# Kernel optimization log

Hardware: AMD Instinct MI355X
Metric: run time of the kernel (lower is better)

## Reference

```python
import jax, jax.numpy as jnp
import numpy as np

CODEBOOK_SIZE = 1024
CODEBOOK_DIM = 64
COMMITMENT_WEIGHT = 0.25
DECAY = 0.99
EPS = 1e-5


def setup_inputs() -> dict:
    key = jax.random.key(0)
    k1, k2, k3 = jax.random.split(key, 3)
    B, D, T = 32, CODEBOOK_DIM, 4096
    z = jax.random.normal(k1, (B, D, T), dtype=jnp.float32)
    embedding = jax.random.normal(k2, (CODEBOOK_SIZE, CODEBOOK_DIM), dtype=jnp.float32)
    cluster_size = jnp.zeros((CODEBOOK_SIZE,), dtype=jnp.float32)
    embed_avg = jax.random.normal(k3, (CODEBOOK_SIZE, CODEBOOK_DIM), dtype=jnp.float32)
    return {"z": z, "embedding": embedding, "cluster_size": cluster_size, "embed_avg": embed_avg}


def reference(z, embedding, cluster_size, embed_avg):
    # z: [B, D, T]; embedding/embed_avg: [K, D]; cluster_size: [K]
    B, D, T = z.shape
    K = embedding.shape[0]
    z_flat = jnp.transpose(z, (0, 2, 1)).reshape(-1, D)  # [N, D], N = B*T

    # squared-euclidean distances via expansion (matches torch cdist expansion)
    dist = (
        jnp.sum(z_flat * z_flat, axis=1, keepdims=True)
        + jnp.sum(embedding * embedding, axis=1)
        - 2.0 * (z_flat @ embedding.T)
    )  # [N, K]
    indices = jnp.argmin(dist, axis=1)  # [N] int

    # EMA updates (training path). one_hot.sum(0) -> segment count; one_hot.T @ z_flat -> segment sum
    counts = jax.ops.segment_sum(jnp.ones(z_flat.shape[0], dtype=z_flat.dtype), indices, num_segments=K)
    new_cluster_size = cluster_size * DECAY + (1.0 - DECAY) * counts
    embed_sum = jax.ops.segment_sum(z_flat, indices, num_segments=K)  # [K, D]
    new_embed_avg = embed_avg * DECAY + (1.0 - DECAY) * embed_sum
    n = jnp.sum(new_cluster_size)
    smoothed = (new_cluster_size + EPS) / (n + K * EPS) * n  # Laplace smoothing
    new_embedding = new_embed_avg / smoothed[:, None]  # [K, D]

    # quantize with the *updated* codebook (as in the torch in-place update)
    z_q_flat = new_embedding[indices]  # [N, D] gather
    loss = COMMITMENT_WEIGHT * jnp.mean((z_flat - jax.lax.stop_gradient(z_q_flat)) ** 2)
    # straight-through estimator
    z_q_flat = z_flat + jax.lax.stop_gradient(z_q_flat - z_flat)
    z_q = jnp.transpose(z_q_flat.reshape(B, T, D), (0, 2, 1))  # [B, D, T]
    return z_q, loss, indices.reshape(B, T)
```

## Files before the change

### kernel.cpp

```cpp
#include <hip/hip_runtime.h>

#define N_PTS 131072
#define TD 4096
#define DD 64
#define KK 1024
#define MARGIN_TH 2e-3f

typedef short bf16x8 __attribute__((ext_vector_type(8)));
typedef float f32x4  __attribute__((ext_vector_type(4)));

__device__ inline unsigned short f2bf(float f) {
    unsigned u = __float_as_uint(f);
    unsigned r = u + 0x7FFFu + ((u >> 16) & 1u);
    return (unsigned short)(r >> 16);
}
__device__ inline float bf2f(unsigned short h) {
    return __uint_as_float(((unsigned)h) << 16);
}

__device__ inline void gload_lds16(const unsigned short* g, unsigned short* l) {
    __builtin_amdgcn_global_load_lds(
        (const __attribute__((address_space(1))) unsigned int*)g,
        (__attribute__((address_space(3))) unsigned int*)l, 16, 0, 0);
}

__global__ __launch_bounds__(256) void vq_prep(const float* __restrict__ z,
                                               unsigned short* __restrict__ zh,
                                               unsigned short* __restrict__ zl)
{
    __shared__ float tile[64][65];
    const int tid = threadIdx.x;
    const int b = blockIdx.x >> 6;
    const int t0 = (blockIdx.x & 63) * 64;

    const int d = tid >> 2, tq = tid & 3;
#pragma unroll
    for (int it = 0; it < 4; ++it) {
        const int tt = tq * 16 + it * 4;
        const float4 v = *(const float4*)(z + ((size_t)b * DD + d) * TD + t0 + tt);
        tile[d][tt] = v.x; tile[d][tt + 1] = v.y; tile[d][tt + 2] = v.z; tile[d][tt + 3] = v.w;
    }
    __syncthreads();

    const int p = tid >> 2, dg = tid & 3;
    bf16x8 h0, h1, l0, l1;
#pragma unroll
    for (int j = 0; j < 8; ++j) {
        const float v0 = -tile[dg * 16 + j][p];
        const unsigned short a = f2bf(v0);
        h0[j] = (short)a; l0[j] = (short)f2bf(v0 - bf2f(a));
        const float v1 = -tile[dg * 16 + 8 + j][p];
        const unsigned short c = f2bf(v1);
        h1[j] = (short)c; l1[j] = (short)f2bf(v1 - bf2f(c));
    }
    const size_t o = ((size_t)(b * TD + t0 + p)) * DD + dg * 16;
    *(bf16x8*)(zh + o) = h0;
    *(bf16x8*)(zh + o + 8) = h1;
    *(bf16x8*)(zl + o) = l0;
    *(bf16x8*)(zl + o + 8) = l1;
}

__global__ __launch_bounds__(256) void vq_eprep(const float* __restrict__ emb,
                                                unsigned short* __restrict__ efh,
                                                unsigned short* __restrict__ efl,
                                                float* __restrict__ halfnorm)
{
    const int k = blockIdx.x * 256 + threadIdx.x;
    if (k >= KK) return;
    const int t = k >> 4, col = k & 15;
    const float* e = emb + (size_t)k * DD;
    double s = 0.0;
#pragma unroll
    for (int d = 0; d < DD; ++d) {
        const float v = e[d];
        const double dv = (double)v;
        s = fma(dv, dv, s);
        const unsigned short h = f2bf(v);
        const int q = d >> 3, j = d & 7;
        const size_t pos = (size_t)t * 1024 + (q >> 2) * 512 + ((q & 3) * 16 + col) * 8 + j;
        efh[pos] = h;
        efl[pos] = f2bf(v - bf2f(h));
    }
    halfnorm[k] = (float)(0.5 * s);
}

__global__ __launch_bounds__(256, 4) void vq_screen_mfma(
    const unsigned short* __restrict__ zh, const unsigned short* __restrict__ zl,
    const unsigned short* __restrict__ efh, const unsigned short* __restrict__ efl,
    const float* __restrict__ hn,
    int* __restrict__ idx_ws, float* __restrict__ ind_out,
    int* __restrict__ nflag, int* __restrict__ flags, int* __restrict__ hist)
{
    __shared__ __align__(16) unsigned short tiles[4][2048];
    __shared__ float hns[KK];

    const int tid  = threadIdx.x;
    const int lane = tid & 63;
    const int wv   = tid >> 6;
    const int quad = lane >> 4;
    const int col  = lane & 15;
    const int loff = lane * 8;
    const int pbase = blockIdx.x * 128 + wv * 32;

    const bf16x8* pA0h = (const bf16x8*)(zh + (size_t)(pbase + col) * DD + quad * 8);
    const bf16x8* pA0l = (const bf16x8*)(zl + (size_t)(pbase + col) * DD + quad * 8);
    const bf16x8* pA1h = (const bf16x8*)(zh + (size_t)(pbase + 16 + col) * DD + quad * 8);
    const bf16x8* pA1l = (const bf16x8*)(zl + (size_t)(pbase + 16 + col) * DD + quad * 8);
    const bf16x8 A0h0 = pA0h[0], A0h1 = pA0h[4];
    const bf16x8 A0l0 = pA0l[0], A0l1 = pA0l[4];
    const bf16x8 A1h0 = pA1h[0], A1h1 = pA1h[4];
    const bf16x8 A1l0 = pA1l[0], A1l1 = pA1l[4];

    ((float4*)hns)[tid] = ((const float4*)hn)[tid];

    const unsigned short* sgl = (wv < 2 ? efh : efl) + (tid & 127) * 8;

    asm volatile("s_waitcnt vmcnt(0)" ::: "memory");
    __builtin_amdgcn_sched_barrier(0);
    __syncthreads();

#define SCREEN_STAGE(T) gload_lds16(sgl + (size_t)(T) * 1024, &tiles[(T) & 3][tid * 8])

    SCREEN_STAGE(0);
    SCREEN_STAGE(1);

    float best0[4]  = {1e30f, 1e30f, 1e30f, 1e30f};
    float best20[4] = {1e30f, 1e30f, 1e30f, 1e30f};
    int   bidx0[4]  = {0, 0, 0, 0};
    float best1[4]  = {1e30f, 1e30f, 1e30f, 1e30f};
    float best21[4] = {1e30f, 1e30f, 1e30f, 1e30f};
    int   bidx1[4]  = {0, 0, 0, 0};

#define SCREEN_BODY(T)                                                              \
    {                                                                               \
        const unsigned short* buf = &tiles[(T) & 3][0];                             \
        const bf16x8 Bh0 = *(const bf16x8*)(buf + loff);                            \
        const bf16x8 Bh1 = *(const bf16x8*)(buf + 512 + loff);                      \
        const bf16x8 Bl0 = *(const bf16x8*)(buf + 1024 + loff);                     \
        const bf16x8 Bl1 = *(const bf16x8*)(buf + 1536 + loff);                     \
        const float chn = hns[(T) * 16 + col];                                      \
        f32x4 a0 = {chn, chn, chn, chn};                                            \
        f32x4 a1 = {chn, chn, chn, chn};                                            \
        a0 = __builtin_amdgcn_mfma_f32_16x16x32_bf16(A0h0, Bh0, a0, 0, 0, 0);       \
        a1 = __builtin_amdgcn_mfma_f32_16x16x32_bf16(A1h0, Bh0, a1, 0, 0, 0);       \
        a0 = __builtin_amdgcn_mfma_f32_16x16x32_bf16(A0h1, Bh1, a0, 0, 0, 0);       \
        a1 = __builtin_amdgcn_mfma_f32_16x16x32_bf16(A1h1, Bh1, a1, 0, 0, 0);       \
        a0 = __builtin_amdgcn_mfma_f32_16x16x32_bf16(A0l0, Bh0, a0, 0, 0, 0);       \
        a1 = __builtin_amdgcn_mfma_f32_16x16x32_bf16(A1l0, Bh0, a1, 0, 0, 0);       \
        a0 = __builtin_amdgcn_mfma_f32_16x16x32_bf16(A0l1, Bh1, a0, 0, 0, 0);       \
        a1 = __builtin_amdgcn_mfma_f32_16x16x32_bf16(A1l1, Bh1, a1, 0, 0, 0);       \
        a0 = __builtin_amdgcn_mfma_f32_16x16x32_bf16(A0h0, Bl0, a0, 0, 0, 0);       \
        a1 = __builtin_amdgcn_mfma_f32_16x16x32_bf16(A1h0, Bl0, a1, 0, 0, 0);       \
        a0 = __builtin_amdgcn_mfma_f32_16x16x32_bf16(A0h1, Bl1, a0, 0, 0, 0);       \
        a1 = __builtin_amdgcn_mfma_f32_16x16x32_bf16(A1h1, Bl1, a1, 0, 0, 0);       \
        const int code = (T) * 16 + col;                                            \
        _Pragma("unroll")                                                           \
        for (int r = 0; r < 4; ++r) {                                               \
            const float s0 = a0[r];                                                 \
            best20[r] = __builtin_amdgcn_fmed3f(best0[r], best20[r], s0);           \
            if (s0 < best0[r]) { best0[r] = s0; bidx0[r] = code; }                  \
            const float s1 = a1[r];                                                 \
            best21[r] = __builtin_amdgcn_fmed3f(best1[r], best21[r], s1);           \
            if (s1 < best1[r]) { best1[r] = s1; bidx1[r] = code; }                  \
        }                                                                           \
    }

    for (int t = 0; t < 62; ++t) {
        SCREEN_STAGE(t + 2);
        asm volatile("s_waitcnt vmcnt(2)" ::: "memory");
        __builtin_amdgcn_sched_barrier(0);
        __builtin_amdgcn_s_barrier();
        __builtin_amdgcn_sched_barrier(0);
        SCREEN_BODY(t);
    }
    asm volatile("s_waitcnt vmcnt(1)" ::: "memory");
    __builtin_amdgcn_sched_barrier(0);
    __builtin_amdgcn_s_barrier();
    __builtin_amdgcn_sched_barrier(0);
    SCREEN_BODY(62);
    asm volatile("s_waitcnt vmcnt(0)" ::: "memory");
    __builtin_amdgcn_sched_barrier(0);
    __builtin_amdgcn_s_barrier();
    __builtin_amdgcn_sched_barrier(0);
    SCREEN_BODY(63);

#undef SCREEN_STAGE
#undef SCREEN_BODY

#pragma unroll
    for (int off = 1; off < 16; off <<= 1) {
#pragma unroll
        for (int r = 0; r < 4; ++r) {
            {
                const float ob  = __shfl_xor(best0[r],  off, 64);
                const float ob2 = __shfl_xor(best20[r], off, 64);
                const int   oi  = __shfl_xor(bidx0[r],  off, 64);
                const float nb2 = fminf(fminf(best20[r], ob2), fmaxf(best0[r], ob));
                if (ob < best0[r]) { best0[r] = ob; bidx0[r] = oi; }
                best20[r] = nb2;
            }
            {
                const float ob  = __shfl_xor(best1[r],  off, 64);
                const float ob2 = __shfl_xor(best21[r], off, 64);
                const int   oi  = __shfl_xor(bidx1[r],  off, 64);
                const float nb2 = fminf(fminf(best21[r], ob2), fmaxf(best1[r], ob));
                if (ob < best1[r]) { best1[r] = ob; bidx1[r] = oi; }
                best21[r] = nb2;
            }
        }
    }

    if (col == 0) {
#pragma unroll
        for (int r = 0; r < 4; ++r) {
            const int n0 = pbase + quad * 4 + r;
            idx_ws[n0] = bidx0[r];
            ind_out[n0] = (float)bidx0[r];
            atomicAdd(&hist[bidx0[r]], 1);
            if (best20[r] - best0[r] < MARGIN_TH) {
                const int pos = atomicAdd(nflag, 1);
                flags[pos] = n0;
            }
            const int n1 = pbase + 16 + quad * 4 + r;
            idx_ws[n1] = bidx1[r];
            ind_out[n1] = (float)bidx1[r];
            atomicAdd(&hist[bidx1[r]], 1);
            if (best21[r] - best1[r] < MARGIN_TH) {
                const int pos = atomicAdd(nflag, 1);
                flags[pos] = n1;
            }
        }
    }
}

__global__ __launch_bounds__(256) void vq_fallback(
    const float* __restrict__ z, const float* __restrict__ emb,
    int* __restrict__ idx_ws, float* __restrict__ ind_out,
    const int* __restrict__ nflag, const int* __restrict__ flags,
    int* __restrict__ hist)
{
    __shared__ float zs[4][DD];
    const int total = *nflag;
    const int lane = threadIdx.x & 63;
    const int wid = threadIdx.x >> 6;
    const int gw = blockIdx.x * 4 + wid;

    for (int i = gw; i < total; i += gridDim.x * 4) {
        const int n = flags[i];
        const int b = n >> 12, t = n & 4095;
        zs[wid][lane] = z[((size_t)b * DD + lane) * TD + t];
        __builtin_amdgcn_s_waitcnt(0);
        double best = 1e300;
        int bi = KK;
        for (int kc = 0; kc < KK / 64; ++kc) {
            const int k = kc * 64 + lane;
            const float4* e = (const float4*)(emb + (size_t)k * DD);
            double dot = 0.0, nn = 0.0;
#pragma unroll
            for (int j = 0; j < 16; ++j) {
                float4 ev = e[j];
                double e0 = (double)ev.x, e1 = (double)ev.y, e2 = (double)ev.z, e3 = (double)ev.w;
                nn = fma(e0, e0, fma(e1, e1, fma(e2, e2, fma(e3, e3, nn))));
                dot = fma((double)zs[wid][4 * j + 0], e0,
                      fma((double)zs[wid][4 * j + 1], e1,
                      fma((double)zs[wid][4 * j + 2], e2,
                      fma((double)zs[wid][4 * j + 3], e3, dot))));
            }
            double s = 0.5 * nn - dot;
            if (s < best || (s == best && k < bi)) { best = s; bi = k; }
        }
        for (int off = 32; off > 0; off >>= 1) {
            double os = __shfl_down(best, off, 64);
            int oi = __shfl_down(bi, off, 64);
            if (os < best || (os == best && oi < bi)) { best = os; bi = oi; }
        }
        if (lane == 0) {
            const int old = idx_ws[n];
            if (bi != old) {
                idx_ws[n] = bi;
                ind_out[n] = (float)bi;
                atomicAdd(&hist[old], -1);
                atomicAdd(&hist[bi], 1);
            }
        }
    }
}

__global__ __launch_bounds__(1024) void vq_prefix_smo(
    const int* __restrict__ hist, const float* __restrict__ cs,
    int* __restrict__ cursor, float* __restrict__ rsmo)
{
    __shared__ int tmp[KK];
    __shared__ double dred[KK];
    const int k = threadIdx.x;
    const int c = hist[k];
    tmp[k] = c;
    const double ncs = 0.99 * (double)cs[k] + 0.01 * (double)c;
    dred[k] = ncs;
    __syncthreads();
    for (int off = 1; off < KK; off <<= 1) {
        int u = (k >= off) ? tmp[k - off] : 0;
        __syncthreads();
        tmp[k] += u;
        __syncthreads();
    }
    cursor[k] = tmp[k] - c;
    for (int s = 512; s > 0; s >>= 1) {
        if (k < s) dred[k] += dred[k + s];
        __syncthreads();
    }
    const double nsum = dred[0];
    const double smo = (ncs + 1e-5) / (nsum + (double)KK * 1e-5) * nsum;
    rsmo[k] = (float)(1.0 / smo);
}

__global__ __launch_bounds__(256) void vq_scatter(const int* __restrict__ idx_ws,
                                                  int* __restrict__ cursor, int* __restrict__ order)
{
    const int n = blockIdx.x * 256 + threadIdx.x;
    const int bi = idx_ws[n];
    const int pos = atomicAdd(&cursor[bi], 1);
    order[pos] = n;
}

__global__ __launch_bounds__(256) void vq_esum2(
    const unsigned short* __restrict__ zh, const unsigned short* __restrict__ zl,
    const int* __restrict__ idx_ws, const int* __restrict__ order,
    float* __restrict__ esum)
{
    const int tid = threadIdx.x;
    const int lane = tid & 63;
    const int w = tid >> 6;
    const int base = blockIdx.x * 256 + w * 64;

    const int pid_l = order[base + lane];
    const int code_l = idx_ws[pid_l];

    float v[64];
#pragma unroll
    for (int j = 0; j < 64; ++j) {
        const int pj = __shfl(pid_l, j, 64);
        const size_t o = (size_t)pj * DD + lane;
        v[j] = bf2f(zh[o]) + bf2f(zl[o]);
    }

    float racc = 0.f;
    int cur = __shfl(code_l, 0, 64);
#pragma unroll
    for (int j = 0; j < 64; ++j) {
        const int cj = __shfl(code_l, j, 64);
        if (cj != cur) {
            atomicAdd(&esum[(size_t)cur * DD + lane], -racc);
            racc = 0.f;
            cur = cj;
        }
        racc += v[j];
    }
    atomicAdd(&esum[(size_t)cur * DD + lane], -racc);
}

__global__ __launch_bounds__(256) void vq_newE(
    const float* __restrict__ avg, const float* __restrict__ esum,
    const float* __restrict__ rsmo, float* __restrict__ newE)
{
    const int j = blockIdx.x * 256 + threadIdx.x;
    newE[j] = (float)((0.99 * (double)avg[j] + 0.01 * (double)esum[j]) * (double)rsmo[j >> 6]);
}

__global__ __launch_bounds__(256) void vq_gather_loss(
    const float* __restrict__ z, const float* __restrict__ newE,
    const int* __restrict__ idx_ws, float* __restrict__ zq_out,
    double* __restrict__ loss_acc, int* __restrict__ done_cnt,
    float* __restrict__ loss_out)
{
    const int tid = threadIdx.x;
    const int n = blockIdx.x * 256 + tid;
    const int b = n >> 12;
    const int t = n & 4095;
    const float* zb = z + ((size_t)b * DD) * TD + t;
    float* ob = zq_out + ((size_t)b * DD) * TD + t;
    const int bi = idx_ws[n];
    const float* e = newE + (size_t)bi * DD;
    double acc = 0.0;
#pragma unroll
    for (int d = 0; d < DD; ++d) {
        float q = e[d];
        float zv = zb[(size_t)d * TD];
        ob[(size_t)d * TD] = q;
        float df = zv - q;
        acc = fma((double)df, (double)df, acc);
    }
    for (int off = 32; off > 0; off >>= 1) acc += __shfl_down(acc, off, 64);
    __shared__ double wsum[4];
    const int wid = tid >> 6, lane = tid & 63;
    if (lane == 0) wsum[wid] = acc;
    __syncthreads();
    if (tid == 0) {
        atomicAdd(loss_acc, wsum[0] + wsum[1] + wsum[2] + wsum[3]);
        __threadfence();
        const int prev = atomicAdd(done_cnt, 1);
        if (prev == gridDim.x - 1) {
            __threadfence();
            *loss_out = (float)(0.25 * (*loss_acc) / (double)(N_PTS * DD));
        }
    }
}

extern "C" void kernel_launch(void* const* d_in, const int* in_sizes, int n_in,
                              void* d_out, int out_size, void* d_ws, size_t ws_size,
                              hipStream_t stream) {
    const float* z    = (const float*)d_in[0];
    const float* emb  = (const float*)d_in[1];
    const float* cs   = (const float*)d_in[2];
    const float* avg  = (const float*)d_in[3];

    float* out      = (float*)d_out;
    float* zq_out   = out;
    float* loss_out = out + 8388608;
    float* ind_out  = out + 8388609;

    unsigned short* zh = (unsigned short*)d_out;
    unsigned short* zl = (unsigned short*)((char*)d_out + 16777216);

    char* ws = (char*)d_ws;
    int*            idx_ws   = (int*)ws;
    float*          newE     = (float*)(ws + 524288);
    float*          esum     = (float*)(ws + 786432);
    int*            hist     = (int*)(ws + 1048576);
    int*            nflag    = (int*)(ws + 1052672);
    int*            done_cnt = (int*)(ws + 1052676);
    double*         loss_acc = (double*)(ws + 1052680);
    float*          halfnorm = (float*)(ws + 1052688);
    int*            cursor   = (int*)(ws + 1056784);
    int*            flags    = (int*)(ws + 1060880);
    int*            order    = (int*)(ws + 1585168);
    unsigned short* efh      = (unsigned short*)(ws + 2109456);
    unsigned short* efl      = (unsigned short*)(ws + 2240528);
    float*          rsmo     = (float*)(ws + 2371600);

    hipMemsetAsync(ws + 786432, 0, 266256, stream);

    vq_prep<<<2048, 256, 0, stream>>>(z, zh, zl);
    vq_eprep<<<4, 256, 0, stream>>>(emb, efh, efl, halfnorm);
    vq_screen_mfma<<<1024, 256, 0, stream>>>(zh, zl, efh, efl, halfnorm,
                                             idx_ws, ind_out, nflag, flags, hist);
    vq_fallback<<<128, 256, 0, stream>>>(z, emb, idx_ws, ind_out, nflag, flags, hist);
    vq_prefix_smo<<<1, 1024, 0, stream>>>(hist, cs, cursor, rsmo);
    vq_scatter<<<N_PTS / 256, 256, 0, stream>>>(idx_ws, cursor, order);
    vq_esum2<<<N_PTS / 256, 256, 0, stream>>>(zh, zl, idx_ws, order, esum);
    vq_newE<<<256, 256, 0, stream>>>(avg, esum, rsmo, newE);
    vq_gather_loss<<<N_PTS / 256, 256, 0, stream>>>(z, newE, idx_ws, zq_out,
                                                    loss_acc, done_cnt, loss_out);
}
```

Before: 342.6 us.

## Merge codebook prep into z prep and build histogram in a separate pass

The codebook prep kernel is folded into vq_prep as four extra blocks, which removes one launch. Those blocks also save the half-norms in double precision, so the fallback no longer recomputes the codebook norms. Per-point global histogram atomics are taken out of the screen and fallback kernels. A new shared-memory histogram kernel runs after the fallback instead. The screen argmin update becomes branchless, and the fallback grid grows from 128 to 1024 blocks. The cost is one extra launch, and dnn shares its workspace region with newE, which is safe only if newE is written after the fallback finishes.

```diff
diff --git a/kernel.cpp b/kernel.cpp
--- a/kernel.cpp
+++ b/kernel.cpp
@@ -26,10 +26,37 @@
 
 __global__ __launch_bounds__(256) void vq_prep(const float* __restrict__ z,
                                                unsigned short* __restrict__ zh,
-                                               unsigned short* __restrict__ zl)
+                                               unsigned short* __restrict__ zl,
+                                               const float* __restrict__ emb,
+                                               unsigned short* __restrict__ efh,
+                                               unsigned short* __restrict__ efl,
+                                               float* __restrict__ halfnorm,
+                                               double* __restrict__ dnn)
 {
     __shared__ float tile[64][65];
     const int tid = threadIdx.x;
+
+    if (blockIdx.x >= 2048) {
+        const int k = (blockIdx.x - 2048) * 256 + tid;
+        const int t = k >> 4, col = k & 15;
+        const float* e = emb + (size_t)k * DD;
+        double s = 0.0;
+#pragma unroll
+        for (int d = 0; d < DD; ++d) {
+            const float v = e[d];
+            const double dv = (double)v;
+            s = fma(dv, dv, s);
+            const unsigned short h = f2bf(v);
+            const int q = d >> 3, j = d & 7;
+            const size_t pos = (size_t)t * 1024 + (q >> 2) * 512 + ((q & 3) * 16 + col) * 8 + j;
+            efh[pos] = h;
+            efl[pos] = f2bf(v - bf2f(h));
+        }
+        halfnorm[k] = (float)(0.5 * s);
+        dnn[k] = 0.5 * s;
+        return;
+    }
+
     const int b = blockIdx.x >> 6;
     const int t0 = (blockIdx.x & 63) * 64;
 
@@ -60,36 +87,12 @@
     *(bf16x8*)(zl + o + 8) = l1;
 }
 
-__global__ __launch_bounds__(256) void vq_eprep(const float* __restrict__ emb,
-                                                unsigned short* __restrict__ efh,
-                                                unsigned short* __restrict__ efl,
-                                                float* __restrict__ halfnorm)
-{
-    const int k = blockIdx.x * 256 + threadIdx.x;
-    if (k >= KK) return;
-    const int t = k >> 4, col = k & 15;
-    const float* e = emb + (size_t)k * DD;
-    double s = 0.0;
-#pragma unroll
-    for (int d = 0; d < DD; ++d) {
-        const float v = e[d];
-        const double dv = (double)v;
-        s = fma(dv, dv, s);
-        const unsigned short h = f2bf(v);
-        const int q = d >> 3, j = d & 7;
-        const size_t pos = (size_t)t * 1024 + (q >> 2) * 512 + ((q & 3) * 16 + col) * 8 + j;
-        efh[pos] = h;
-        efl[pos] = f2bf(v - bf2f(h));
-    }
-    halfnorm[k] = (float)(0.5 * s);
-}
-
 __global__ __launch_bounds__(256, 4) void vq_screen_mfma(
     const unsigned short* __restrict__ zh, const unsigned short* __restrict__ zl,
     const unsigned short* __restrict__ efh, const unsigned short* __restrict__ efl,
     const float* __restrict__ hn,
     int* __restrict__ idx_ws, float* __restrict__ ind_out,
-    int* __restrict__ nflag, int* __restrict__ flags, int* __restrict__ hist)
+    int* __restrict__ nflag, int* __restrict__ flags)
 {
     __shared__ __align__(16) unsigned short tiles[4][2048];
     __shared__ float hns[KK];
@@ -102,27 +105,27 @@
     const int loff = lane * 8;
     const int pbase = blockIdx.x * 128 + wv * 32;
 
-    const bf16x8* pA0h = (const bf16x8*)(zh + (size_t)(pbase + col) * DD + quad * 8);
-    const bf16x8* pA0l = (const bf16x8*)(zl + (size_t)(pbase + col) * DD + quad * 8);
-    const bf16x8* pA1h = (const bf16x8*)(zh + (size_t)(pbase + 16 + col) * DD + quad * 8);
-    const bf16x8* pA1l = (const bf16x8*)(zl + (size_t)(pbase + 16 + col) * DD + quad * 8);
-    const bf16x8 A0h0 = pA0h[0], A0h1 = pA0h[4];
-    const bf16x8 A0l0 = pA0l[0], A0l1 = pA0l[4];
-    const bf16x8 A1h0 = pA1h[0], A1h1 = pA1h[4];
-    const bf16x8 A1l0 = pA1l[0], A1l1 = pA1l[4];
+    const bf16x8* ph0 = (const bf16x8*)(zh + (size_t)(pbase + col) * DD + quad * 8);
+    const bf16x8* pl0 = (const bf16x8*)(zl + (size_t)(pbase + col) * DD + quad * 8);
+    const bf16x8* ph1 = (const bf16x8*)(zh + (size_t)(pbase + 16 + col) * DD + quad * 8);
+    const bf16x8* pl1 = (const bf16x8*)(zl + (size_t)(pbase + 16 + col) * DD + quad * 8);
+    const bf16x8 A0h0 = ph0[0], A0h1 = ph0[4];
+    const bf16x8 A0l0 = pl0[0], A0l1 = pl0[4];
+    const bf16x8 A1h0 = ph1[0], A1h1 = ph1[4];
+    const bf16x8 A1l0 = pl1[0], A1l1 = pl1[4];
 
     ((float4*)hns)[tid] = ((const float4*)hn)[tid];
 
-    const unsigned short* sgl = (wv < 2 ? efh : efl) + (tid & 127) * 8;
+    const unsigned short* sg = (tid < 128) ? (efh + tid * 8) : (efl + (tid - 128) * 8);
 
     asm volatile("s_waitcnt vmcnt(0)" ::: "memory");
     __builtin_amdgcn_sched_barrier(0);
     __syncthreads();
 
-#define SCREEN_STAGE(T) gload_lds16(sgl + (size_t)(T) * 1024, &tiles[(T) & 3][tid * 8])
-
-    SCREEN_STAGE(0);
-    SCREEN_STAGE(1);
+#define STAGE(T) gload_lds16(sg + (size_t)(T) * 1024, &tiles[(T) & 3][tid * 8])
+
+    STAGE(0);
+    STAGE(1);
 
     float best0[4]  = {1e30f, 1e30f, 1e30f, 1e30f};
     float best20[4] = {1e30f, 1e30f, 1e30f, 1e30f};
@@ -131,7 +134,7 @@
     float best21[4] = {1e30f, 1e30f, 1e30f, 1e30f};
     int   bidx1[4]  = {0, 0, 0, 0};
 
-#define SCREEN_BODY(T)                                                              \
+#define BODY(T)                                                                     \
     {                                                                               \
         const unsigned short* buf = &tiles[(T) & 3][0];                             \
         const bf16x8 Bh0 = *(const bf16x8*)(buf + loff);                            \
@@ -158,34 +161,36 @@
         for (int r = 0; r < 4; ++r) {                                               \
             const float s0 = a0[r];                                                 \
             best20[r] = __builtin_amdgcn_fmed3f(best0[r], best20[r], s0);           \
-            if (s0 < best0[r]) { best0[r] = s0; bidx0[r] = code; }                  \
+            bidx0[r] = (s0 < best0[r]) ? code : bidx0[r];                           \
+            best0[r] = fminf(best0[r], s0);                                         \
             const float s1 = a1[r];                                                 \
             best21[r] = __builtin_amdgcn_fmed3f(best1[r], best21[r], s1);           \
-            if (s1 < best1[r]) { best1[r] = s1; bidx1[r] = code; }                  \
+            bidx1[r] = (s1 < best1[r]) ? code : bidx1[r];                           \
+            best1[r] = fminf(best1[r], s1);                                         \
         }                                                                           \
     }
 
     for (int t = 0; t < 62; ++t) {
-        SCREEN_STAGE(t + 2);
+        STAGE(t + 2);
         asm volatile("s_waitcnt vmcnt(2)" ::: "memory");
         __builtin_amdgcn_sched_barrier(0);
         __builtin_amdgcn_s_barrier();
         __builtin_amdgcn_sched_barrier(0);
-        SCREEN_BODY(t);
+        BODY(t);
     }
     asm volatile("s_waitcnt vmcnt(1)" ::: "memory");
     __builtin_amdgcn_sched_barrier(0);
     __builtin_amdgcn_s_barrier();
     __builtin_amdgcn_sched_barrier(0);
-    SCREEN_BODY(62);
+    BODY(62);
     asm volatile("s_waitcnt vmcnt(0)" ::: "memory");
     __builtin_amdgcn_sched_barrier(0);
     __builtin_amdgcn_s_barrier();
     __builtin_amdgcn_sched_barrier(0);
-    SCREEN_BODY(63);
-
-#undef SCREEN_STAGE
-#undef SCREEN_BODY
+    BODY(63);
+
+#undef STAGE
+#undef BODY
 
 #pragma unroll
     for (int off = 1; off < 16; off <<= 1) {
@@ -216,7 +221,6 @@
             const int n0 = pbase + quad * 4 + r;
             idx_ws[n0] = bidx0[r];
             ind_out[n0] = (float)bidx0[r];
-            atomicAdd(&hist[bidx0[r]], 1);
             if (best20[r] - best0[r] < MARGIN_TH) {
                 const int pos = atomicAdd(nflag, 1);
                 flags[pos] = n0;
@@ -224,7 +228,6 @@
             const int n1 = pbase + 16 + quad * 4 + r;
             idx_ws[n1] = bidx1[r];
             ind_out[n1] = (float)bidx1[r];
-            atomicAdd(&hist[bidx1[r]], 1);
             if (best21[r] - best1[r] < MARGIN_TH) {
                 const int pos = atomicAdd(nflag, 1);
                 flags[pos] = n1;
@@ -235,9 +238,9 @@
 
 __global__ __launch_bounds__(256) void vq_fallback(
     const float* __restrict__ z, const float* __restrict__ emb,
+    const double* __restrict__ dnn,
     int* __restrict__ idx_ws, float* __restrict__ ind_out,
-    const int* __restrict__ nflag, const int* __restrict__ flags,
-    int* __restrict__ hist)
+    const int* __restrict__ nflag, const int* __restrict__ flags)
 {
     __shared__ float zs[4][DD];
     const int total = *nflag;
@@ -255,18 +258,16 @@
         for (int kc = 0; kc < KK / 64; ++kc) {
             const int k = kc * 64 + lane;
             const float4* e = (const float4*)(emb + (size_t)k * DD);
-            double dot = 0.0, nn = 0.0;
+            double dot = 0.0;
 #pragma unroll
             for (int j = 0; j < 16; ++j) {
                 float4 ev = e[j];
-                double e0 = (double)ev.x, e1 = (double)ev.y, e2 = (double)ev.z, e3 = (double)ev.w;
-                nn = fma(e0, e0, fma(e1, e1, fma(e2, e2, fma(e3, e3, nn))));
-                dot = fma((double)zs[wid][4 * j + 0], e0,
-                      fma((double)zs[wid][4 * j + 1], e1,
-                      fma((double)zs[wid][4 * j + 2], e2,
-                      fma((double)zs[wid][4 * j + 3], e3, dot))));
+                dot = fma((double)zs[wid][4 * j + 0], (double)ev.x,
+                      fma((double)zs[wid][4 * j + 1], (double)ev.y,
+                      fma((double)zs[wid][4 * j + 2], (double)ev.z,
+                      fma((double)zs[wid][4 * j + 3], (double)ev.w, dot))));
             }
-            double s = 0.5 * nn - dot;
+            double s = dnn[k] - dot;
             if (s < best || (s == best && k < bi)) { best = s; bi = k; }
         }
         for (int off = 32; off > 0; off >>= 1) {
@@ -274,16 +275,22 @@
             int oi = __shfl_down(bi, off, 64);
             if (os < best || (os == best && oi < bi)) { best = os; bi = oi; }
         }
-        if (lane == 0) {
-            const int old = idx_ws[n];
-            if (bi != old) {
-                idx_ws[n] = bi;
-                ind_out[n] = (float)bi;
-                atomicAdd(&hist[old], -1);
-                atomicAdd(&hist[bi], 1);
-            }
-        }
-    }
+        if (lane == 0) { idx_ws[n] = bi; ind_out[n] = (float)bi; }
+    }
+}
+
+__global__ __launch_bounds__(256) void vq_hist(const int* __restrict__ idx_ws, int* __restrict__ hist)
+{
+    __shared__ int h[KK];
+    for (int i = threadIdx.x; i < KK; i += 256) h[i] = 0;
+    __syncthreads();
+    const int base = blockIdx.x * 2048;
+#pragma unroll
+    for (int j = 0; j < 8; ++j)
+        atomicAdd(&h[idx_ws[base + j * 256 + threadIdx.x]], 1);
+    __syncthreads();
+    for (int i = threadIdx.x; i < KK; i += 256)
+        if (h[i]) atomicAdd(&hist[i], h[i]);
 }
 
 __global__ __launch_bounds__(1024) void vq_prefix_smo(
@@ -425,6 +432,7 @@
     char* ws = (char*)d_ws;
     int*            idx_ws   = (int*)ws;
     float*          newE     = (float*)(ws + 524288);
+    double*         dnn      = (double*)(ws + 524288);
     float*          esum     = (float*)(ws + 786432);
     int*            hist     = (int*)(ws + 1048576);
     int*            nflag    = (int*)(ws + 1052672);
@@ -440,11 +448,11 @@
 
     hipMemsetAsync(ws + 786432, 0, 266256, stream);
 
-    vq_prep<<<2048, 256, 0, stream>>>(z, zh, zl);
-    vq_eprep<<<4, 256, 0, stream>>>(emb, efh, efl, halfnorm);
-    vq_screen_mfma<<<1024, 256, 0, stream>>>(zh, zl, efh, efl, halfnorm,
-                                             idx_ws, ind_out, nflag, flags, hist);
-    vq_fallback<<<128, 256, 0, stream>>>(z, emb, idx_ws, ind_out, nflag, flags, hist);
+    vq_prep<<<2052, 256, 0, stream>>>(z, zh, zl, emb, efh, efl, halfnorm, dnn);
+    vq_screen_mfma<<<N_PTS / 128, 256, 0, stream>>>(zh, zl, efh, efl, halfnorm,
+                                                    idx_ws, ind_out, nflag, flags);
+    vq_fallback<<<1024, 256, 0, stream>>>(z, emb, dnn, idx_ws, ind_out, nflag, flags);
+    vq_hist<<<64, 256, 0, stream>>>(idx_ws, hist);
     vq_prefix_smo<<<1, 1024, 0, stream>>>(hist, cs, cursor, rsmo);
     vq_scatter<<<N_PTS / 256, 256, 0, stream>>>(idx_ws, cursor, order);
     vq_esum2<<<N_PTS / 256, 256, 0, stream>>>(zh, zl, idx_ws, order, esum);
```

After: 288.2 us. 15.9% less time.
